# Optimization experiments

Hardware: AMD Instinct MI355X
Metric: run time of the kernel (lower is better)

The kernel has to match this reference:

```python
import jax, jax.numpy as jnp
import numpy as np

D_MODEL = 128
REDUCTION = 4
KSIZE = 3
B = D_MODEL  # required by the original code's groups=B conv shape constraint
L = 4096


def setup_inputs() -> dict:
    key = jax.random.key(0)
    ks = jax.random.split(key, 7)
    d, r, K = D_MODEL, REDUCTION, KSIZE
    return {
        "x": jax.random.normal(ks[0], (B, L, d), dtype=jnp.float32),
        "W1": jax.random.normal(ks[1], (d // r, d), dtype=jnp.float32) * (1.0 / np.sqrt(d)),
        "b1": jax.random.normal(ks[2], (d // r,), dtype=jnp.float32) * 0.01,
        "W2": jax.random.normal(ks[3], (K, d // r), dtype=jnp.float32) * (1.0 / np.sqrt(d // r)),
        "b2": jax.random.normal(ks[4], (K,), dtype=jnp.float32) * 0.01,
        "Wc": jax.random.normal(ks[5], (d, d), dtype=jnp.float32) * (1.0 / np.sqrt(d)),
        "bc": jax.random.normal(ks[6], (d,), dtype=jnp.float32) * 0.01,
    }


def reference(x, W1, b1, W2, b2, Wc, bc):
    # x: [B, L, d] with B == d (required by original groups=B conv)
    Bsz, Lseq, d = x.shape
    K = W2.shape[0]
    pad = (K - 1) // 2
    # kernel generation from global average pool
    m = x.mean(axis=1)                                   # [B, d]
    h = jax.nn.gelu(m @ W1.T + b1, approximate=False)    # [B, d//r]
    w = jax.nn.softmax(h @ W2.T + b2, axis=-1)           # [B, K]; row j is the kernel for channel j
    # depthwise-style cross-correlation: y[b, l, c] = sum_k xp[b, l+k, c] * w[c, k]
    xp = jnp.pad(x, ((0, 0), (pad, pad), (0, 0)))        # [B, L+2*pad, d]
    y = sum(xp[:, k:k + Lseq, :] * w[None, None, :, k] for k in range(K))  # [B, L, d]
    # pointwise conv (kernel_size=1) == per-token linear
    return y @ Wc.T + bc                                 # [B, L, d]
```

## Files before the change

kernel.cpp:

```cpp
#include <hip/hip_runtime.h>
#include <hip/hip_bf16.h>

#define D_MODEL 128
#define SEQ_L   4096
#define BATCH   128
#define TM      128
#define NSEG    8
#define YPAD    132

typedef float f4 __attribute__((ext_vector_type(4)));
typedef float f32x4 __attribute__((ext_vector_type(4)));
typedef short bf16x8 __attribute__((ext_vector_type(8)));

__device__ __forceinline__ unsigned short f2bf(float f) {
    union { float f; unsigned u; } v; v.f = f;
    unsigned r = v.u + 0x7FFFu + ((v.u >> 16) & 1u);
    return (unsigned short)(r >> 16);
}

__global__ __launch_bounds__(512) void kmean(const float* __restrict__ x,
                                             float* __restrict__ part) {
    int seg = blockIdx.x, b = blockIdx.y;
    int t = threadIdx.x;
    int c4 = t & 31, ph = t >> 5;
    const f4* xb = reinterpret_cast<const f4*>(x + (size_t)b * SEQ_L * D_MODEL);
    int l0 = seg * (SEQ_L / NSEG);

    f4 a0 = {0.f,0.f,0.f,0.f}, a1 = a0, a2 = a0, a3 = a0;
    #pragma unroll
    for (int i = 0; i < 32; i += 4) {
        a0 += xb[(l0 + ph + (i + 0) * 16) * 32 + c4];
        a1 += xb[(l0 + ph + (i + 1) * 16) * 32 + c4];
        a2 += xb[(l0 + ph + (i + 2) * 16) * 32 + c4];
        a3 += xb[(l0 + ph + (i + 3) * 16) * 32 + c4];
    }
    f4 acc = (a0 + a1) + (a2 + a3);

    __shared__ f4 red[512];
    red[t] = acc;
    __syncthreads();
    if (t < 32) {
        f4 s = red[t];
        #pragma unroll
        for (int p = 1; p < 16; ++p) s += red[t + 32 * p];
        reinterpret_cast<f4*>(part + ((size_t)b * NSEG + seg) * D_MODEL)[t] = s;
    }
}

__global__ __launch_bounds__(128) void kweights(const float* __restrict__ part,
                                                const float* __restrict__ W1,
                                                const float* __restrict__ b1,
                                                const float* __restrict__ W2,
                                                const float* __restrict__ b2,
                                                float* __restrict__ w) {
    int c = threadIdx.x;
    f4 mv[32];
    #pragma unroll
    for (int d4 = 0; d4 < 32; ++d4) mv[d4] = (f4){0.f, 0.f, 0.f, 0.f};
    for (int s = 0; s < NSEG; ++s) {
        const f4* ps = reinterpret_cast<const f4*>(part + ((size_t)c * NSEG + s) * D_MODEL);
        #pragma unroll
        for (int d4 = 0; d4 < 32; ++d4) mv[d4] += ps[d4];
    }
    #pragma unroll
    for (int d4 = 0; d4 < 32; ++d4) mv[d4] *= (1.0f / (float)SEQ_L);

    float h[32];
    #pragma unroll
    for (int j = 0; j < 32; ++j) {
        const f4* w1r = reinterpret_cast<const f4*>(W1 + j * 128);
        f4 s4 = {0.f, 0.f, 0.f, 0.f};
        #pragma unroll
        for (int d4 = 0; d4 < 32; ++d4) s4 += mv[d4] * w1r[d4];
        float s = s4[0] + s4[1] + s4[2] + s4[3] + b1[j];
        h[j] = 0.5f * s * (1.0f + erff(s * 0.70710678118654752f));
    }
    float lg[3];
    float mx = -1e30f;
    #pragma unroll
    for (int k = 0; k < 3; ++k) {
        float s = b2[k];
        #pragma unroll
        for (int j = 0; j < 32; ++j) s += h[j] * W2[k * 32 + j];
        lg[k] = s;
        mx = fmaxf(mx, s);
    }
    float e[3], den = 0.f;
    #pragma unroll
    for (int k = 0; k < 3; ++k) { e[k] = __expf(lg[k] - mx); den += e[k]; }
    float inv = 1.0f / den;
    #pragma unroll
    for (int k = 0; k < 3; ++k) w[k * 128 + c] = e[k] * inv;
}

__global__ __launch_bounds__(256) void kcvt(const float* __restrict__ Wc,
                                            unsigned short* __restrict__ wcb) {
    int i = blockIdx.x * 256 + threadIdx.x;
    f4 v = reinterpret_cast<const f4*>(Wc)[i];
    ushort4 o;
    o.x = f2bf(v[0]); o.y = f2bf(v[1]); o.z = f2bf(v[2]); o.w = f2bf(v[3]);
    reinterpret_cast<ushort4*>(wcb)[i] = o;
}

__global__ __launch_bounds__(512, 4) void kconv(const float* __restrict__ x,
                                                const float* __restrict__ w,
                                                const unsigned short* __restrict__ wcb,
                                                const float* __restrict__ bc,
                                                float* __restrict__ out) {
    __shared__ __align__(16) unsigned short y_lds[TM][YPAD];

    int t = threadIdx.x;
    int b = blockIdx.y;
    int l0 = blockIdx.x * TM;
    const float* xb = x + (size_t)b * SEQ_L * D_MODEL;

    int lane = t & 63, wid = t >> 6;
    int co0 = wid * 16;
    int arow = co0 + (lane & 15);
    int kb = (lane >> 4) * 8;

    bf16x8 awc[4];
    #pragma unroll
    for (int kc = 0; kc < 4; ++kc)
        awc[kc] = *reinterpret_cast<const bf16x8*>(wcb + (size_t)arow * 128 + kc * 32 + kb);

    int c4 = t & 31;
    f4 w0 = reinterpret_cast<const f4*>(w)[c4];
    f4 w1 = reinterpret_cast<const f4*>(w + 128)[c4];
    f4 w2 = reinterpret_cast<const f4*>(w + 256)[c4];

    {
        int rg = t >> 5;
        int r0 = rg * 8;
        int lb = l0 + r0;
        f4 prev = (lb > 0) ? reinterpret_cast<const f4*>(xb + (size_t)(lb - 1) * D_MODEL)[c4]
                           : (f4){0.f, 0.f, 0.f, 0.f};
        f4 cur = reinterpret_cast<const f4*>(xb + (size_t)lb * D_MODEL)[c4];
        #pragma unroll
        for (int i = 0; i < 8; ++i) {
            int l = lb + i;
            f4 nxt = (l < SEQ_L - 1)
                         ? reinterpret_cast<const f4*>(xb + (size_t)(l + 1) * D_MODEL)[c4]
                         : (f4){0.f, 0.f, 0.f, 0.f};
            f4 y = prev * w0 + cur * w1 + nxt * w2;
            ushort4 yb;
            yb.x = f2bf(y[0]); yb.y = f2bf(y[1]); yb.z = f2bf(y[2]); yb.w = f2bf(y[3]);
            *reinterpret_cast<ushort4*>(&y_lds[r0 + i][c4 * 4]) = yb;
            prev = cur;
            cur = nxt;
        }
    }
    __syncthreads();

    f32x4 acc[8];
    #pragma unroll
    for (int tt = 0; tt < 8; ++tt) acc[tt] = (f32x4){0.f, 0.f, 0.f, 0.f};

    #pragma unroll
    for (int tt = 0; tt < 8; ++tt) {
        #pragma unroll
        for (int kc = 0; kc < 4; ++kc) {
            bf16x8 by = *reinterpret_cast<const bf16x8*>(&y_lds[tt * 16 + (lane & 15)][kc * 32 + kb]);
            acc[tt] = __builtin_amdgcn_mfma_f32_16x16x32_bf16(awc[kc], by, acc[tt], 0, 0, 0);
        }
    }

    int cb = (lane >> 4) * 4;
    f4 bcv = *reinterpret_cast<const f4*>(bc + co0 + cb);
    #pragma unroll
    for (int tt = 0; tt < 8; ++tt) {
        int l = l0 + tt * 16 + (lane & 15);
        f4 v = acc[tt] + bcv;
        *reinterpret_cast<f4*>(out + ((size_t)b * SEQ_L + l) * D_MODEL + co0 + cb) = v;
    }
}

extern "C" void kernel_launch(void* const* d_in, const int* in_sizes, int n_in,
                              void* d_out, int out_size, void* d_ws, size_t ws_size,
                              hipStream_t stream) {
    const float* x  = (const float*)d_in[0];
    const float* W1 = (const float*)d_in[1];
    const float* b1 = (const float*)d_in[2];
    const float* W2 = (const float*)d_in[3];
    const float* b2 = (const float*)d_in[4];
    const float* Wc = (const float*)d_in[5];
    const float* bc = (const float*)d_in[6];
    float* out = (float*)d_out;

    char* ws = (char*)d_ws;
    float* part = (float*)ws;
    float* w    = (float*)(ws + 524288);
    unsigned short* wcb = (unsigned short*)(ws + 526336);

    kmean<<<dim3(NSEG, BATCH), 512, 0, stream>>>(x, part);
    kweights<<<1, 128, 0, stream>>>(part, W1, b1, W2, b2, w);
    kcvt<<<16, 256, 0, stream>>>(Wc, wcb);
    kconv<<<dim3(SEQ_L / TM, BATCH), 512, 0, stream>>>(x, w, wcb, bc, out);
}
```

Baseline: 251.9 us.

## Compute conv directly into MFMA registers, drop LDS staging, fold Wc cast into mean kernel

The conv kernel no longer stages the depthwise-filtered tile in LDS. Each wave now loads the x rows it needs straight from global memory, computes the 3-tap filter, packs the result to bf16 and feeds it to MFMA over a 64-token by 64-channel tile, using 256-thread blocks. The separate Wc-to-bf16 conversion kernel is merged into extra blocks of the mean kernel, which removes one launch. The cost is redundant global loads: each x row is read three times, and each wave pair reads the same x. More registers are also live for the 4x4 accumulator tile.

```diff
diff --git a/kernel.cpp b/kernel.cpp
--- a/kernel.cpp
+++ b/kernel.cpp
@@ -4,9 +4,7 @@
 #define D_MODEL 128
 #define SEQ_L   4096
 #define BATCH   128
-#define TM      128
 #define NSEG    8
-#define YPAD    132
 
 typedef float f4 __attribute__((ext_vector_type(4)));
 typedef float f32x4 __attribute__((ext_vector_type(4)));
@@ -19,7 +17,19 @@
 }
 
 __global__ __launch_bounds__(512) void kmean(const float* __restrict__ x,
-                                             float* __restrict__ part) {
+                                             float* __restrict__ part,
+                                             const float* __restrict__ Wc,
+                                             unsigned short* __restrict__ wcb) {
+    if (blockIdx.x == NSEG) {
+        if (blockIdx.y < 8) {
+            int i = blockIdx.y * 512 + threadIdx.x;
+            f4 v = reinterpret_cast<const f4*>(Wc)[i];
+            ushort4 o;
+            o.x = f2bf(v[0]); o.y = f2bf(v[1]); o.z = f2bf(v[2]); o.w = f2bf(v[3]);
+            reinterpret_cast<ushort4*>(wcb)[i] = o;
+        }
+        return;
+    }
     int seg = blockIdx.x, b = blockIdx.y;
     int t = threadIdx.x;
     int c4 = t & 31, ph = t >> 5;
@@ -93,86 +103,106 @@
     for (int k = 0; k < 3; ++k) w[k * 128 + c] = e[k] * inv;
 }
 
-__global__ __launch_bounds__(256) void kcvt(const float* __restrict__ Wc,
-                                            unsigned short* __restrict__ wcb) {
-    int i = blockIdx.x * 256 + threadIdx.x;
-    f4 v = reinterpret_cast<const f4*>(Wc)[i];
-    ushort4 o;
-    o.x = f2bf(v[0]); o.y = f2bf(v[1]); o.z = f2bf(v[2]); o.w = f2bf(v[3]);
-    reinterpret_cast<ushort4*>(wcb)[i] = o;
-}
-
-__global__ __launch_bounds__(512, 4) void kconv(const float* __restrict__ x,
-                                                const float* __restrict__ w,
+template<bool GUARD>
+__device__ __forceinline__ void tile64(const float* __restrict__ xb,
+                                       const float* __restrict__ wv,
+                                       const unsigned short* __restrict__ wcb,
+                                       const float* __restrict__ bc,
+                                       float* __restrict__ outb,
+                                       int tokbase, int lane, int co0w) {
+    const int r = lane & 15, q = lane >> 4;
+    const int kb = q * 8;
+
+    f32x4 acc[4][4];
+    #pragma unroll
+    for (int g = 0; g < 4; ++g)
+        #pragma unroll
+        for (int n = 0; n < 4; ++n) acc[g][n] = (f32x4){0.f, 0.f, 0.f, 0.f};
+
+    #pragma unroll
+    for (int kc = 0; kc < 4; ++kc) {
+        const int off = kc * 32 + kb;
+
+        bf16x8 awc[4];
+        #pragma unroll
+        for (int n = 0; n < 4; ++n)
+            awc[n] = *reinterpret_cast<const bf16x8*>(
+                wcb + (size_t)(co0w + n * 16 + r) * D_MODEL + off);
+
+        f4 w0a = *reinterpret_cast<const f4*>(wv + off);
+        f4 w0b = *reinterpret_cast<const f4*>(wv + off + 4);
+        f4 w1a = *reinterpret_cast<const f4*>(wv + 128 + off);
+        f4 w1b = *reinterpret_cast<const f4*>(wv + 128 + off + 4);
+        f4 w2a = *reinterpret_cast<const f4*>(wv + 256 + off);
+        f4 w2b = *reinterpret_cast<const f4*>(wv + 256 + off + 4);
+
+        #pragma unroll
+        for (int g = 0; g < 4; ++g) {
+            int tok = tokbase + g * 16 + r;
+            const float* xrow = xb + (size_t)tok * D_MODEL;
+            const float* rm = xrow - D_MODEL;
+            const float* rp = xrow + D_MODEL;
+            bool gm = true, gp = true;
+            if (GUARD) {
+                gm = tok > 0; gp = tok < SEQ_L - 1;
+                rm = gm ? rm : xrow;
+                rp = gp ? rp : xrow;
+            }
+            f4 xma = *reinterpret_cast<const f4*>(rm + off);
+            f4 xmb = *reinterpret_cast<const f4*>(rm + off + 4);
+            f4 x0a = *reinterpret_cast<const f4*>(xrow + off);
+            f4 x0b = *reinterpret_cast<const f4*>(xrow + off + 4);
+            f4 xpa = *reinterpret_cast<const f4*>(rp + off);
+            f4 xpb = *reinterpret_cast<const f4*>(rp + off + 4);
+            if (GUARD) {
+                f4 z = {0.f, 0.f, 0.f, 0.f};
+                if (!gm) { xma = z; xmb = z; }
+                if (!gp) { xpa = z; xpb = z; }
+            }
+            f4 y0 = xma * w0a + x0a * w1a + xpa * w2a;
+            f4 y1 = xmb * w0b + x0b * w1b + xpb * w2b;
+            bf16x8 pv;
+            pv[0] = (short)f2bf(y0[0]);
+            pv[1] = (short)f2bf(y0[1]);
+            pv[2] = (short)f2bf(y0[2]);
+            pv[3] = (short)f2bf(y0[3]);
+            pv[4] = (short)f2bf(y1[0]);
+            pv[5] = (short)f2bf(y1[1]);
+            pv[6] = (short)f2bf(y1[2]);
+            pv[7] = (short)f2bf(y1[3]);
+            #pragma unroll
+            for (int n = 0; n < 4; ++n)
+                acc[g][n] = __builtin_amdgcn_mfma_f32_16x16x32_bf16(awc[n], pv, acc[g][n], 0, 0, 0);
+        }
+    }
+
+    #pragma unroll
+    for (int g = 0; g < 4; ++g) {
+        int tok = tokbase + g * 16 + r;
+        float* orow = outb + (size_t)tok * D_MODEL + co0w + q * 4;
+        #pragma unroll
+        for (int n = 0; n < 4; ++n) {
+            f4 bcv = *reinterpret_cast<const f4*>(bc + co0w + n * 16 + q * 4);
+            *reinterpret_cast<f4*>(orow + n * 16) = acc[g][n] + bcv;
+        }
+    }
+}
+
+__global__ __launch_bounds__(256, 2) void kconv(const float* __restrict__ x,
+                                                const float* __restrict__ wv,
                                                 const unsigned short* __restrict__ wcb,
                                                 const float* __restrict__ bc,
                                                 float* __restrict__ out) {
-    __shared__ __align__(16) unsigned short y_lds[TM][YPAD];
-
-    int t = threadIdx.x;
+    int t = threadIdx.x, lane = t & 63, w = t >> 6;
     int b = blockIdx.y;
-    int l0 = blockIdx.x * TM;
+    int tokbase = blockIdx.x * 128 + (w >> 1) * 64;
+    int co0w = (w & 1) * 64;
     const float* xb = x + (size_t)b * SEQ_L * D_MODEL;
-
-    int lane = t & 63, wid = t >> 6;
-    int co0 = wid * 16;
-    int arow = co0 + (lane & 15);
-    int kb = (lane >> 4) * 8;
-
-    bf16x8 awc[4];
-    #pragma unroll
-    for (int kc = 0; kc < 4; ++kc)
-        awc[kc] = *reinterpret_cast<const bf16x8*>(wcb + (size_t)arow * 128 + kc * 32 + kb);
-
-    int c4 = t & 31;
-    f4 w0 = reinterpret_cast<const f4*>(w)[c4];
-    f4 w1 = reinterpret_cast<const f4*>(w + 128)[c4];
-    f4 w2 = reinterpret_cast<const f4*>(w + 256)[c4];
-
-    {
-        int rg = t >> 5;
-        int r0 = rg * 8;
-        int lb = l0 + r0;
-        f4 prev = (lb > 0) ? reinterpret_cast<const f4*>(xb + (size_t)(lb - 1) * D_MODEL)[c4]
-                           : (f4){0.f, 0.f, 0.f, 0.f};
-        f4 cur = reinterpret_cast<const f4*>(xb + (size_t)lb * D_MODEL)[c4];
-        #pragma unroll
-        for (int i = 0; i < 8; ++i) {
-            int l = lb + i;
-            f4 nxt = (l < SEQ_L - 1)
-                         ? reinterpret_cast<const f4*>(xb + (size_t)(l + 1) * D_MODEL)[c4]
-                         : (f4){0.f, 0.f, 0.f, 0.f};
-            f4 y = prev * w0 + cur * w1 + nxt * w2;
-            ushort4 yb;
-            yb.x = f2bf(y[0]); yb.y = f2bf(y[1]); yb.z = f2bf(y[2]); yb.w = f2bf(y[3]);
-            *reinterpret_cast<ushort4*>(&y_lds[r0 + i][c4 * 4]) = yb;
-            prev = cur;
-            cur = nxt;
-        }
-    }
-    __syncthreads();
-
-    f32x4 acc[8];
-    #pragma unroll
-    for (int tt = 0; tt < 8; ++tt) acc[tt] = (f32x4){0.f, 0.f, 0.f, 0.f};
-
-    #pragma unroll
-    for (int tt = 0; tt < 8; ++tt) {
-        #pragma unroll
-        for (int kc = 0; kc < 4; ++kc) {
-            bf16x8 by = *reinterpret_cast<const bf16x8*>(&y_lds[tt * 16 + (lane & 15)][kc * 32 + kb]);
-            acc[tt] = __builtin_amdgcn_mfma_f32_16x16x32_bf16(awc[kc], by, acc[tt], 0, 0, 0);
-        }
-    }
-
-    int cb = (lane >> 4) * 4;
-    f4 bcv = *reinterpret_cast<const f4*>(bc + co0 + cb);
-    #pragma unroll
-    for (int tt = 0; tt < 8; ++tt) {
-        int l = l0 + tt * 16 + (lane & 15);
-        f4 v = acc[tt] + bcv;
-        *reinterpret_cast<f4*>(out + ((size_t)b * SEQ_L + l) * D_MODEL + co0 + cb) = v;
-    }
+    float* outb = out + (size_t)b * SEQ_L * D_MODEL;
+    if (blockIdx.x == 0 || blockIdx.x == (SEQ_L / 128) - 1)
+        tile64<true>(xb, wv, wcb, bc, outb, tokbase, lane, co0w);
+    else
+        tile64<false>(xb, wv, wcb, bc, outb, tokbase, lane, co0w);
 }
 
 extern "C" void kernel_launch(void* const* d_in, const int* in_sizes, int n_in,
@@ -192,8 +222,7 @@
     float* w    = (float*)(ws + 524288);
     unsigned short* wcb = (unsigned short*)(ws + 526336);
 
-    kmean<<<dim3(NSEG, BATCH), 512, 0, stream>>>(x, part);
+    kmean<<<dim3(NSEG + 1, BATCH), 512, 0, stream>>>(x, part, Wc, wcb);
     kweights<<<1, 128, 0, stream>>>(part, W1, b1, W2, b2, w);
-    kcvt<<<16, 256, 0, stream>>>(Wc, wcb);
-    kconv<<<dim3(SEQ_L / TM, BATCH), 512, 0, stream>>>(x, w, wcb, bc, out);
-}
+    kconv<<<dim3(SEQ_L / 128, BATCH), 256, 0, stream>>>(x, w, wcb, bc, out);
+}
```

After: 390.4 us. +55.0%, slower.

## Fold Wc conversion into mean kernel and pipeline conv over double-buffered chunks

Applied to the files above, without the earlier changes.

Removes the separate Wc-to-bf16 conversion launch by giving the mean kernel an extra column of blocks that does the conversion. The conv kernel now handles 256 tokens per block in four 64-token chunks with double-buffered LDS, prefetching the next chunk's x rows into registers while MFMAs run on the current one. This amortizes the Wc fragment and weight loads over more tokens and overlaps global loads with compute. In exchange it halves the grid, lowers the occupancy hint to 2, and adds two barriers per chunk.

```diff
diff --git a/kernel.cpp b/kernel.cpp
--- a/kernel.cpp
+++ b/kernel.cpp
@@ -4,9 +4,7 @@
 #define D_MODEL 128
 #define SEQ_L   4096
 #define BATCH   128
-#define TM      128
 #define NSEG    8
-#define YPAD    132
 
 typedef float f4 __attribute__((ext_vector_type(4)));
 typedef float f32x4 __attribute__((ext_vector_type(4)));
@@ -19,7 +17,19 @@
 }
 
 __global__ __launch_bounds__(512) void kmean(const float* __restrict__ x,
-                                             float* __restrict__ part) {
+                                             float* __restrict__ part,
+                                             const float* __restrict__ Wc,
+                                             unsigned short* __restrict__ wcb) {
+    if (blockIdx.x == NSEG) {
+        if (blockIdx.y < 8) {
+            int i = blockIdx.y * 512 + threadIdx.x;
+            f4 v = reinterpret_cast<const f4*>(Wc)[i];
+            ushort4 o;
+            o.x = f2bf(v[0]); o.y = f2bf(v[1]); o.z = f2bf(v[2]); o.w = f2bf(v[3]);
+            reinterpret_cast<ushort4*>(wcb)[i] = o;
+        }
+        return;
+    }
     int seg = blockIdx.x, b = blockIdx.y;
     int t = threadIdx.x;
     int c4 = t & 31, ph = t >> 5;
@@ -93,85 +103,91 @@
     for (int k = 0; k < 3; ++k) w[k * 128 + c] = e[k] * inv;
 }
 
-__global__ __launch_bounds__(256) void kcvt(const float* __restrict__ Wc,
-                                            unsigned short* __restrict__ wcb) {
-    int i = blockIdx.x * 256 + threadIdx.x;
-    f4 v = reinterpret_cast<const f4*>(Wc)[i];
-    ushort4 o;
-    o.x = f2bf(v[0]); o.y = f2bf(v[1]); o.z = f2bf(v[2]); o.w = f2bf(v[3]);
-    reinterpret_cast<ushort4*>(wcb)[i] = o;
-}
-
-__global__ __launch_bounds__(512, 4) void kconv(const float* __restrict__ x,
-                                                const float* __restrict__ w,
+template<bool GUARD>
+__device__ __forceinline__ void load6(const float* __restrict__ xb, int gr0, int c4, f4 R[6]) {
+    #pragma unroll
+    for (int j = 0; j < 6; ++j) {
+        int gr = gr0 + j;
+        if (GUARD) {
+            bool ok = (gr >= 0) && (gr < SEQ_L);
+            int grc = ok ? gr : 0;
+            f4 v = reinterpret_cast<const f4*>(xb + (size_t)grc * D_MODEL)[c4];
+            f4 z = {0.f, 0.f, 0.f, 0.f};
+            R[j] = ok ? v : z;
+        } else {
+            R[j] = reinterpret_cast<const f4*>(xb + (size_t)gr * D_MODEL)[c4];
+        }
+    }
+}
+
+__global__ __launch_bounds__(512, 2) void kconv(const float* __restrict__ x,
+                                                const float* __restrict__ wv,
                                                 const unsigned short* __restrict__ wcb,
                                                 const float* __restrict__ bc,
                                                 float* __restrict__ out) {
-    __shared__ __align__(16) unsigned short y_lds[TM][YPAD];
+    __shared__ __align__(16) unsigned short y_lds[2][64][132];
 
     int t = threadIdx.x;
     int b = blockIdx.y;
-    int l0 = blockIdx.x * TM;
+    int base = blockIdx.x * 256;
     const float* xb = x + (size_t)b * SEQ_L * D_MODEL;
-
+    float* outb = out + (size_t)b * SEQ_L * D_MODEL;
+
+    int c4 = t & 31, rg = t >> 5;
     int lane = t & 63, wid = t >> 6;
+    int r = lane & 15, q = lane >> 4, kb = q * 8;
     int co0 = wid * 16;
-    int arow = co0 + (lane & 15);
-    int kb = (lane >> 4) * 8;
+
+    f4 w0 = reinterpret_cast<const f4*>(wv)[c4];
+    f4 w1 = reinterpret_cast<const f4*>(wv + 128)[c4];
+    f4 w2 = reinterpret_cast<const f4*>(wv + 256)[c4];
 
     bf16x8 awc[4];
     #pragma unroll
     for (int kc = 0; kc < 4; ++kc)
-        awc[kc] = *reinterpret_cast<const bf16x8*>(wcb + (size_t)arow * 128 + kc * 32 + kb);
-
-    int c4 = t & 31;
-    f4 w0 = reinterpret_cast<const f4*>(w)[c4];
-    f4 w1 = reinterpret_cast<const f4*>(w + 128)[c4];
-    f4 w2 = reinterpret_cast<const f4*>(w + 256)[c4];
-
-    {
-        int rg = t >> 5;
-        int r0 = rg * 8;
-        int lb = l0 + r0;
-        f4 prev = (lb > 0) ? reinterpret_cast<const f4*>(xb + (size_t)(lb - 1) * D_MODEL)[c4]
-                           : (f4){0.f, 0.f, 0.f, 0.f};
-        f4 cur = reinterpret_cast<const f4*>(xb + (size_t)lb * D_MODEL)[c4];
-        #pragma unroll
-        for (int i = 0; i < 8; ++i) {
-            int l = lb + i;
-            f4 nxt = (l < SEQ_L - 1)
-                         ? reinterpret_cast<const f4*>(xb + (size_t)(l + 1) * D_MODEL)[c4]
-                         : (f4){0.f, 0.f, 0.f, 0.f};
-            f4 y = prev * w0 + cur * w1 + nxt * w2;
+        awc[kc] = *reinterpret_cast<const bf16x8*>(wcb + (size_t)(co0 + r) * D_MODEL + kc * 32 + kb);
+
+    f4 bcv = *reinterpret_cast<const f4*>(bc + co0 + q * 4);
+
+    f4 R[6];
+    if (base == 0) load6<true>(xb, base + rg * 4 - 1, c4, R);
+    else           load6<false>(xb, base + rg * 4 - 1, c4, R);
+
+    #pragma unroll
+    for (int i = 0; i < 4; ++i) {
+        int buf = i & 1;
+        #pragma unroll
+        for (int j = 0; j < 4; ++j) {
+            f4 y = R[j] * w0 + R[j + 1] * w1 + R[j + 2] * w2;
             ushort4 yb;
             yb.x = f2bf(y[0]); yb.y = f2bf(y[1]); yb.z = f2bf(y[2]); yb.w = f2bf(y[3]);
-            *reinterpret_cast<ushort4*>(&y_lds[r0 + i][c4 * 4]) = yb;
-            prev = cur;
-            cur = nxt;
-        }
-    }
-    __syncthreads();
-
-    f32x4 acc[8];
-    #pragma unroll
-    for (int tt = 0; tt < 8; ++tt) acc[tt] = (f32x4){0.f, 0.f, 0.f, 0.f};
-
-    #pragma unroll
-    for (int tt = 0; tt < 8; ++tt) {
-        #pragma unroll
-        for (int kc = 0; kc < 4; ++kc) {
-            bf16x8 by = *reinterpret_cast<const bf16x8*>(&y_lds[tt * 16 + (lane & 15)][kc * 32 + kb]);
-            acc[tt] = __builtin_amdgcn_mfma_f32_16x16x32_bf16(awc[kc], by, acc[tt], 0, 0, 0);
-        }
-    }
-
-    int cb = (lane >> 4) * 4;
-    f4 bcv = *reinterpret_cast<const f4*>(bc + co0 + cb);
-    #pragma unroll
-    for (int tt = 0; tt < 8; ++tt) {
-        int l = l0 + tt * 16 + (lane & 15);
-        f4 v = acc[tt] + bcv;
-        *reinterpret_cast<f4*>(out + ((size_t)b * SEQ_L + l) * D_MODEL + co0 + cb) = v;
+            *reinterpret_cast<ushort4*>(&y_lds[buf][rg * 4 + j][c4 * 4]) = yb;
+        }
+        if (i < 3) {
+            int ntok0 = base + (i + 1) * 64;
+            if (ntok0 + 64 == SEQ_L) load6<true>(xb, ntok0 + rg * 4 - 1, c4, R);
+            else                     load6<false>(xb, ntok0 + rg * 4 - 1, c4, R);
+        }
+        __syncthreads();
+
+        f32x4 acc[4];
+        #pragma unroll
+        for (int g = 0; g < 4; ++g) acc[g] = (f32x4){0.f, 0.f, 0.f, 0.f};
+        #pragma unroll
+        for (int g = 0; g < 4; ++g)
+            #pragma unroll
+            for (int kc = 0; kc < 4; ++kc) {
+                bf16x8 bv = *reinterpret_cast<const bf16x8*>(&y_lds[buf][g * 16 + r][kc * 32 + kb]);
+                acc[g] = __builtin_amdgcn_mfma_f32_16x16x32_bf16(awc[kc], bv, acc[g], 0, 0, 0);
+            }
+
+        int tokt = base + i * 64;
+        #pragma unroll
+        for (int g = 0; g < 4; ++g) {
+            int tok = tokt + g * 16 + r;
+            *reinterpret_cast<f4*>(outb + (size_t)tok * D_MODEL + co0 + q * 4) = acc[g] + bcv;
+        }
+        __syncthreads();
     }
 }
 
@@ -192,8 +208,7 @@
     float* w    = (float*)(ws + 524288);
     unsigned short* wcb = (unsigned short*)(ws + 526336);
 
-    kmean<<<dim3(NSEG, BATCH), 512, 0, stream>>>(x, part);
+    kmean<<<dim3(NSEG + 1, BATCH), 512, 0, stream>>>(x, part, Wc, wcb);
     kweights<<<1, 128, 0, stream>>>(part, W1, b1, W2, b2, w);
-    kcvt<<<16, 256, 0, stream>>>(Wc, wcb);
-    kconv<<<dim3(SEQ_L / TM, BATCH), 512, 0, stream>>>(x, w, wcb, bc, out);
-}
+    kconv<<<dim3(SEQ_L / 256, BATCH), 512, 0, stream>>>(x, w, wcb, bc, out);
+}
```

Result: faster. 235.7 us (-6.4%).
